# Kernel tuning notes

Measured on AMD Instinct MI355X. Metric: run time of the kernel, lower is better.

Reference implementation:

```python
import jax, jax.numpy as jnp
import numpy as np
from jax import lax

B, T, C_IN, HW = 16, 2048, 17, 8
N_CONV, HID, OUT = 4, 150, 2
IN_SZ = N_CONV * 6 * 6  # 144


def setup_inputs() -> dict:
    key = jax.random.key(0)
    ks = jax.random.split(key, 9)
    s = lambda *sh: 1.0 / np.sqrt(sh[-1])
    return {
        "inputs": jax.random.normal(ks[0], (B, T, C_IN, HW, HW), jnp.float32),
        "conv_w": jax.random.normal(ks[1], (N_CONV, C_IN, 3, 3), jnp.float32) * 0.1,
        "conv_b": jax.random.normal(ks[2], (N_CONV,), jnp.float32) * 0.1,
        "w_ih": jax.random.normal(ks[3], (4 * HID, IN_SZ), jnp.float32) * s(IN_SZ),
        "w_hh": jax.random.normal(ks[4], (4 * HID, HID), jnp.float32) * s(HID),
        "b_ih": jax.random.normal(ks[5], (4 * HID,), jnp.float32) * s(HID),
        "b_hh": jax.random.normal(ks[6], (4 * HID,), jnp.float32) * s(HID),
        "last_w": jax.random.normal(ks[7], (OUT, HID), jnp.float32) * s(HID),
        "last_b": jax.random.normal(ks[8], (OUT,), jnp.float32) * s(HID),
    }


def reference(inputs, conv_w, conv_b, w_ih, w_hh, b_ih, b_hh, last_w, last_b):
    b, t = inputs.shape[:2]
    # Conv2d over all timesteps at once (same math as the per-step loop).
    x = inputs.reshape(b * t, C_IN, HW, HW)
    y = lax.conv_general_dilated(
        x, conv_w, window_strides=(1, 1), padding="VALID",
        dimension_numbers=("NCHW", "OIHW", "NCHW"),
    ) + conv_b[None, :, None, None]           # [B*T, 4, 6, 6]
    y = jax.nn.relu(y).reshape(b, t, IN_SZ)   # [B, T, 144]
    # Precompute input-to-gate projection for every step (batched GEMM).
    gates_x = jnp.einsum("btf,gf->btg", y, w_ih) + b_ih + b_hh  # [B, T, 600]

    def step(carry, gx):
        h, c = carry
        g = gx + h @ w_hh.T  # [B, 600]; PyTorch gate order: i, f, g, o
        i, f, gg, o = jnp.split(g, 4, axis=-1)
        c = jax.nn.sigmoid(f) * c + jax.nn.sigmoid(i) * jnp.tanh(gg)
        h = jax.nn.sigmoid(o) * jnp.tanh(c)
        return (h, c), None

    h0 = jnp.zeros((b, HID), inputs.dtype)
    (hT, _), _ = lax.scan(step, (h0, h0), jnp.swapaxes(gates_x, 0, 1))
    return hT @ last_w.T + last_b  # [B, 2] == last(h_T).squeeze()
```

## Files before the change

### kernel.cpp

```cpp
#include <hip/hip_runtime.h>

typedef _Float16 f16;
typedef _Float16 f16x4 __attribute__((ext_vector_type(4)));
typedef _Float16 f16x8 __attribute__((ext_vector_type(8)));
typedef float f32x4 __attribute__((ext_vector_type(4)));
typedef int i32x4 __attribute__((ext_vector_type(4)));

#define TLEN 2048
#define TPAD 2050
#define NCOL 640
#define GSTEP (16 * NCOL)
#define SPITCH 1099
#define K1 1.4426950408889634f
#define K2 2.8853900817779268f

__global__ __launch_bounds__(64) void rowmax_k(const float* __restrict__ w_hh,
                                               float* __restrict__ rowmax)
{
    const int r = blockIdx.x * 64 + threadIdx.x;
    if (r < 600) {
        float m = 0.f;
        for (int k = 0; k < 150; ++k) m = fmaxf(m, fabsf(w_hh[r * 150 + k]));
        rowmax[r] = m;
    }
}

__global__ void prep_weights(const float* __restrict__ w_ih,
                             const float* __restrict__ w_hh,
                             const float* __restrict__ b_ih,
                             const float* __restrict__ b_hh,
                             const float* __restrict__ rowmax,
                             f16* __restrict__ wihf, signed char* __restrict__ whhq,
                             float* __restrict__ biasp, float* __restrict__ dsc)
{
    const int idx = blockIdx.x * blockDim.x + threadIdx.x;
    const int stride = gridDim.x * blockDim.x;
    for (int i = idx; i < 40 * 5 * 64 * 8; i += stride) {
        const int e = i & 7;
        const int lane = (i >> 3) & 63;
        const int kt = (i >> 9) % 5;
        const int nt = i / 2560;
        const int colg = nt * 16 + (lane & 15);
        const int u = colg >> 2, G = colg & 3;
        const int k = kt * 32 + (lane >> 4) * 8 + e;
        const float sc = (G == 2) ? K2 : -K1;
        f16 vi = (f16)0.f;
        if (u < 150 && k < 144) vi = (f16)(w_ih[(G * 150 + u) * 144 + k] * sc);
        wihf[i] = vi;
    }
    for (int i = idx; i < 40 * 3 * 64 * 16; i += stride) {
        const int byte = i & 15;
        const int lane = (i >> 4) & 63;
        const int kt = (i >> 10) % 3;
        const int nt = i / 3072;
        const int colg = nt * 16 + (lane & 15);
        const int u = colg >> 2, G = colg & 3;
        const int k = kt * 64 + (lane >> 4) * 16 + byte;
        signed char q = 0;
        if (u < 150 && k < 150) {
            const int row = G * 150 + u;
            const float rm = rowmax[row];
            if (rm > 0.f)
                q = (signed char)(int)rintf(w_hh[row * 150 + k] * (127.f / rm));
        }
        whhq[i] = q;
    }
    for (int i = idx; i < NCOL; i += stride) {
        const int u = i >> 2, G = i & 3;
        const float sc = (G == 2) ? K2 : -K1;
        biasp[i] = (u < 150) ? (b_ih[G * 150 + u] + b_hh[G * 150 + u]) * sc : 0.f;
        dsc[i]   = (u < 150) ? sc * rowmax[G * 150 + u] * (1.f / 16129.f) : 0.f;
    }
}

__global__ __launch_bounds__(512, 1) void conv_gemm(
    const float* __restrict__ inp, const float* __restrict__ cw,
    const float* __restrict__ cb,
    const f16* __restrict__ wihf, const float* __restrict__ biasp,
    f16* __restrict__ gates3)
{
    __shared__ float s_in[16][SPITCH];
    __shared__ __align__(16) f16 s_y[8][16][168];
    __shared__ float s_w[612];
    const int tid = threadIdx.x, w = tid >> 6, lane = tid & 63;
    const int col = lane & 15, grp = lane >> 4;
    for (int i = tid; i < 612; i += 512) s_w[i] = cw[i];

    f16x8 bfr[5][5];
    float bb[5];
    #pragma unroll
    for (int i = 0; i < 5; ++i) {
        const int nt = w * 5 + i;
        const f16* wf = wihf + (size_t)(nt * 5) * 512;
        #pragma unroll
        for (int kt = 0; kt < 5; ++kt)
            bfr[i][kt] = *(const f16x8*)(wf + kt * 512 + lane * 8);
        bb[i] = biasp[nt * 16 + col];
    }
    const int cb_b = tid & 15, unit = tid >> 4;
    const int oc = unit / 6, oy = unit % 6;
    const float cbias = (unit < 24) ? cb[oc] : 0.f;
    __syncthreads();

    const int t0 = blockIdx.x * 8;
    for (int tl = 0; tl < 8; ++tl) {
        const int t = t0 + tl;
        __syncthreads();
        {
            const int si = tid >> 5, l2 = tid & 31;
            const float* ip = inp + ((size_t)si * TLEN + t) * 1088;
            for (int k = l2; k < 1088; k += 32) s_in[si][k] = ip[k];
        }
        __syncthreads();
        if (unit < 24) {
            const float* wp = s_w + oc * 153;
            float acc[6] = {cbias, cbias, cbias, cbias, cbias, cbias};
            #pragma unroll 1
            for (int ic = 0; ic < 17; ++ic) {
                const float* rowb = &s_in[cb_b][ic * 64 + oy * 8];
                #pragma unroll
                for (int ky = 0; ky < 3; ++ky) {
                    const float* r = rowb + ky * 8;
                    const float w0 = wp[ic * 9 + ky * 3 + 0];
                    const float w1 = wp[ic * 9 + ky * 3 + 1];
                    const float w2 = wp[ic * 9 + ky * 3 + 2];
                    #pragma unroll
                    for (int ox = 0; ox < 6; ++ox)
                        acc[ox] += r[ox] * w0 + r[ox + 1] * w1 + r[ox + 2] * w2;
                }
            }
            #pragma unroll
            for (int ox = 0; ox < 6; ++ox)
                s_y[tl][cb_b][oc * 36 + oy * 6 + ox] = (f16)fmaxf(acc[ox], 0.f);
        } else if (unit == 24) {
            #pragma unroll
            for (int k = 0; k < 16; ++k) s_y[tl][cb_b][144 + k] = (f16)0.f;
        }
    }
    __syncthreads();
    for (int tl = 0; tl < 8; ++tl) {
        const int t = t0 + tl;
        f16x8 a[5];
        #pragma unroll
        for (int kt = 0; kt < 5; ++kt)
            a[kt] = *(const f16x8*)(&s_y[tl][col][kt * 32 + grp * 8]);
        #pragma unroll
        for (int i = 0; i < 5; ++i) {
            f32x4 acc = {0.f, 0.f, 0.f, 0.f};
            #pragma unroll
            for (int kt = 0; kt < 5; ++kt)
                acc = __builtin_amdgcn_mfma_f32_16x16x32_f16(a[kt], bfr[i][kt], acc, 0, 0, 0);
            const int colg = (w * 5 + i) * 16 + col;
            #pragma unroll
            for (int r = 0; r < 4; ++r)
                gates3[((size_t)(t * 16 + grp * 4 + r)) * NCOL + colg] =
                    (f16)(acc[r] + bb[i]);
        }
    }
}

__device__ __forceinline__ void lstm_stepQ(
    int t, int cur, f16x4& pfu, f16x4& pfc, const f16*& pLoad,
    const i32x4 (&afrag)[5][3], const f32x4& scv,
    signed char* hqs, f16* hfs, float& cst,
    int grp, int sel, bool wr, int u)
{
    const f16x4 pnew = *(const f16x4*)pLoad;
    pLoad += GSTEP;

    const signed char* hr = hqs + cur * 192 + grp * 16;
    i32x4 bf[3];
    #pragma unroll
    for (int kt = 0; kt < 3; ++kt)
        bf[kt] = *(const i32x4*)(hr + kt * 64);

    float gx0 = (float)pfu[0], gx1 = (float)pfu[1];
    float gx2 = (float)pfu[2], gx3 = (float)pfu[3];
    pfc = pnew;

    const i32x4 zc = {0, 0, 0, 0};
    i32x4 acc[5];
    #pragma unroll
    for (int i = 0; i < 5; ++i)
        acc[i] = __builtin_amdgcn_mfma_i32_16x16x64_i8(afrag[i][0], bf[0], zc, 0, 0, 0);
    #pragma unroll
    for (int kt = 1; kt < 3; ++kt)
        #pragma unroll
        for (int i = 0; i < 5; ++i)
            acc[i] = __builtin_amdgcn_mfma_i32_16x16x64_i8(afrag[i][kt], bf[kt], acc[i], 0, 0, 0);

    int s0 = acc[0][0], s1 = acc[0][1], s2 = acc[0][2], s3 = acc[0][3];
    #pragma unroll
    for (int i = 1; i < 5; ++i) {
        const bool p = (sel == i);
        s0 = p ? acc[i][0] : s0;
        s1 = p ? acc[i][1] : s1;
        s2 = p ? acc[i][2] : s2;
        s3 = p ? acc[i][3] : s3;
    }

    const float g0 = fmaf((float)s0, scv[0], gx0);
    const float g1 = fmaf((float)s1, scv[1], gx1);
    const float g2 = fmaf((float)s2, scv[2], gx2);
    const float g3 = fmaf((float)s3, scv[3], gx3);

    const float ei = __builtin_amdgcn_exp2f(g0);
    const float ef = __builtin_amdgcn_exp2f(g1);
    const float eg = __builtin_amdgcn_exp2f(fminf(g2, 38.f));
    const float eo = __builtin_amdgcn_exp2f(g3);
    const float dig = (1.f + ei) * (eg + 1.f);
    const float c = cst * __builtin_amdgcn_rcpf(1.f + ef)
                  + (eg - 1.f) * __builtin_amdgcn_rcpf(dig);
    cst = c;
    const float ec = __builtin_amdgcn_exp2f(fminf(K2 * c, 80.f));
    const float h = (ec - 1.f) * __builtin_amdgcn_rcpf((1.f + eo) * (ec + 1.f));

    if (wr) hqs[(cur ^ 1) * 192 + u] = (signed char)(int)rintf(127.f * h);
    if (t == TLEN - 1 && wr) hfs[u] = (f16)h;

    asm volatile("s_waitcnt lgkmcnt(0)" ::: "memory");
    __builtin_amdgcn_s_barrier();
    __builtin_amdgcn_sched_barrier(0);
}

__global__ __launch_bounds__(512, 1) void lstm_scan(
    const f16* __restrict__ gates3, const signed char* __restrict__ whhq,
    const float* __restrict__ dsc,
    const float* __restrict__ last_w, const float* __restrict__ last_b,
    float* __restrict__ out)
{
    __shared__ __align__(16) signed char hq[2 * 192];
    __shared__ __align__(16) f16 hf[160];
    const int b = blockIdx.x;
    const int tid = threadIdx.x, w = tid >> 6, lane = tid & 63;
    const int col = lane & 15, grp = lane >> 4;
    const int sel = (col < 5) ? col : ((col < 10) ? col - 5 : ((col < 15) ? col - 10 : 0));
    const bool wr = (col < 5);
    const int u = 20 * w + 4 * sel + grp;

    for (int i = tid; i < 2 * 192; i += 512) hq[i] = 0;

    i32x4 afrag[5][3];
    #pragma unroll
    for (int i = 0; i < 5; ++i)
        #pragma unroll
        for (int kt = 0; kt < 3; ++kt)
            afrag[i][kt] =
                *(const i32x4*)(whhq + (size_t)(((5 * w + i) * 3 + kt) * 64 + lane) * 16);

    const f32x4 scv = *(const f32x4*)(dsc + 4 * u);
    float cst = 0.f;
    __syncthreads();

    const f16* gbu = gates3 + (size_t)b * NCOL + 80 * w + 16 * sel + 4 * grp;
    f16x4 pA = *(const f16x4*)(gbu);
    f16x4 pB = *(const f16x4*)(gbu + (size_t)1 * GSTEP);
    const f16* pLoad = gbu + (size_t)2 * GSTEP;

    #pragma unroll 1
    for (int tb = 0; tb < TLEN; tb += 2) {
        lstm_stepQ(tb,     0, pA, pA, pLoad, afrag, scv, hq, hf, cst, grp, sel, wr, u);
        lstm_stepQ(tb + 1, 1, pB, pB, pLoad, afrag, scv, hq, hf, cst, grp, sel, wr, u);
    }

    if (tid < 2) {
        float s = last_b[tid];
        for (int j = 0; j < 150; ++j)
            s += (float)hf[j] * last_w[tid * 150 + j];
        out[b * 2 + tid] = s;
    }
}

extern "C" void kernel_launch(void* const* d_in, const int* in_sizes, int n_in,
                              void* d_out, int out_size, void* d_ws, size_t ws_size,
                              hipStream_t stream) {
    const float* inp    = (const float*)d_in[0];
    const float* conv_w = (const float*)d_in[1];
    const float* conv_b = (const float*)d_in[2];
    const float* w_ih   = (const float*)d_in[3];
    const float* w_hh   = (const float*)d_in[4];
    const float* b_ih   = (const float*)d_in[5];
    const float* b_hh   = (const float*)d_in[6];
    const float* last_w = (const float*)d_in[7];
    const float* last_b = (const float*)d_in[8];
    float* out = (float*)d_out;

    char* ws = (char*)d_ws;
    size_t off = 0;
    f16*   gates3 = (f16*)(ws + off);  off += (size_t)TPAD * 16 * NCOL * 2;
    f16*   wihf   = (f16*)(ws + off);  off += 204800;
    signed char* whhq = (signed char*)(ws + off); off += 122880;
    float* biasp  = (float*)(ws + off); off += 2560;
    float* dsc    = (float*)(ws + off); off += 2560;
    float* rowmax = (float*)(ws + off); off += 2560;

    rowmax_k<<<10, 64, 0, stream>>>(w_hh, rowmax);
    prep_weights<<<120, 256, 0, stream>>>(w_ih, w_hh, b_ih, b_hh, rowmax,
                                          wihf, whhq, biasp, dsc);
    conv_gemm<<<256, 512, 0, stream>>>(inp, conv_w, conv_b, wihf, biasp, gates3);
    lstm_scan<<<16, 512, 0, stream>>>(gates3, whhq, dsc, last_w, last_b, out);
}
```

Before: 1.004 ms.

## Fold weight prep kernels into conv_gemm and lstm_scan, vectorize conv loads

Removes the separate rowmax and weight-prep launches. Each conv_gemm block now converts w_ih and the biases to f16 fragments itself, and each lstm_scan block computes the w_hh row maxima and int8-quantizes its fragments on entry. This saves two kernel launches and the workspace round trips. The conv input staging and the stencil reads switch to float4 accesses, with the shared pitch padded to 1100 to keep 16-byte alignment. The cost is redundant weight conversion in every block, which adds latency at the start of the serial LSTM kernel, and a possible rise in shared-memory bank conflicts from the new pitch.

```diff
diff --git a/kernel.cpp b/kernel.cpp
--- a/kernel.cpp
+++ b/kernel.cpp
@@ -10,76 +10,18 @@
 #define TPAD 2050
 #define NCOL 640
 #define GSTEP (16 * NCOL)
-#define SPITCH 1099
+#define SPITCH 1100
 #define K1 1.4426950408889634f
 #define K2 2.8853900817779268f
-
-__global__ __launch_bounds__(64) void rowmax_k(const float* __restrict__ w_hh,
-                                               float* __restrict__ rowmax)
-{
-    const int r = blockIdx.x * 64 + threadIdx.x;
-    if (r < 600) {
-        float m = 0.f;
-        for (int k = 0; k < 150; ++k) m = fmaxf(m, fabsf(w_hh[r * 150 + k]));
-        rowmax[r] = m;
-    }
-}
-
-__global__ void prep_weights(const float* __restrict__ w_ih,
-                             const float* __restrict__ w_hh,
-                             const float* __restrict__ b_ih,
-                             const float* __restrict__ b_hh,
-                             const float* __restrict__ rowmax,
-                             f16* __restrict__ wihf, signed char* __restrict__ whhq,
-                             float* __restrict__ biasp, float* __restrict__ dsc)
-{
-    const int idx = blockIdx.x * blockDim.x + threadIdx.x;
-    const int stride = gridDim.x * blockDim.x;
-    for (int i = idx; i < 40 * 5 * 64 * 8; i += stride) {
-        const int e = i & 7;
-        const int lane = (i >> 3) & 63;
-        const int kt = (i >> 9) % 5;
-        const int nt = i / 2560;
-        const int colg = nt * 16 + (lane & 15);
-        const int u = colg >> 2, G = colg & 3;
-        const int k = kt * 32 + (lane >> 4) * 8 + e;
-        const float sc = (G == 2) ? K2 : -K1;
-        f16 vi = (f16)0.f;
-        if (u < 150 && k < 144) vi = (f16)(w_ih[(G * 150 + u) * 144 + k] * sc);
-        wihf[i] = vi;
-    }
-    for (int i = idx; i < 40 * 3 * 64 * 16; i += stride) {
-        const int byte = i & 15;
-        const int lane = (i >> 4) & 63;
-        const int kt = (i >> 10) % 3;
-        const int nt = i / 3072;
-        const int colg = nt * 16 + (lane & 15);
-        const int u = colg >> 2, G = colg & 3;
-        const int k = kt * 64 + (lane >> 4) * 16 + byte;
-        signed char q = 0;
-        if (u < 150 && k < 150) {
-            const int row = G * 150 + u;
-            const float rm = rowmax[row];
-            if (rm > 0.f)
-                q = (signed char)(int)rintf(w_hh[row * 150 + k] * (127.f / rm));
-        }
-        whhq[i] = q;
-    }
-    for (int i = idx; i < NCOL; i += stride) {
-        const int u = i >> 2, G = i & 3;
-        const float sc = (G == 2) ? K2 : -K1;
-        biasp[i] = (u < 150) ? (b_ih[G * 150 + u] + b_hh[G * 150 + u]) * sc : 0.f;
-        dsc[i]   = (u < 150) ? sc * rowmax[G * 150 + u] * (1.f / 16129.f) : 0.f;
-    }
-}
 
 __global__ __launch_bounds__(512, 1) void conv_gemm(
     const float* __restrict__ inp, const float* __restrict__ cw,
     const float* __restrict__ cb,
-    const f16* __restrict__ wihf, const float* __restrict__ biasp,
+    const float* __restrict__ w_ih, const float* __restrict__ b_ih,
+    const float* __restrict__ b_hh,
     f16* __restrict__ gates3)
 {
-    __shared__ float s_in[16][SPITCH];
+    __shared__ __align__(16) float s_in[16][SPITCH];
     __shared__ __align__(16) f16 s_y[8][16][168];
     __shared__ float s_w[612];
     const int tid = threadIdx.x, w = tid >> 6, lane = tid & 63;
@@ -90,13 +32,27 @@
     float bb[5];
     #pragma unroll
     for (int i = 0; i < 5; ++i) {
-        const int nt = w * 5 + i;
-        const f16* wf = wihf + (size_t)(nt * 5) * 512;
-        #pragma unroll
-        for (int kt = 0; kt < 5; ++kt)
-            bfr[i][kt] = *(const f16x8*)(wf + kt * 512 + lane * 8);
-        bb[i] = biasp[nt * 16 + col];
-    }
+        const int colg = (w * 5 + i) * 16 + col;
+        const int u = colg >> 2, G = colg & 3;
+        const float sc = (G == 2) ? K2 : -K1;
+        const bool valid = (u < 150);
+        const int row = valid ? G * 150 + u : 0;
+        #pragma unroll
+        for (int kt = 0; kt < 5; ++kt) {
+            const int k0 = kt * 32 + grp * 8;
+            f16x8 v;
+            #pragma unroll
+            for (int e = 0; e < 8; ++e) v[e] = (f16)0.f;
+            if (valid && k0 < 144) {
+                const float* p = w_ih + (size_t)row * 144 + k0;
+                #pragma unroll
+                for (int e = 0; e < 8; ++e) v[e] = (f16)(p[e] * sc);
+            }
+            bfr[i][kt] = v;
+        }
+        bb[i] = valid ? (b_ih[row] + b_hh[row]) * sc : 0.f;
+    }
+
     const int cb_b = tid & 15, unit = tid >> 4;
     const int oc = unit / 6, oy = unit % 6;
     const float cbias = (unit < 24) ? cb[oc] : 0.f;
@@ -108,8 +64,10 @@
         __syncthreads();
         {
             const int si = tid >> 5, l2 = tid & 31;
-            const float* ip = inp + ((size_t)si * TLEN + t) * 1088;
-            for (int k = l2; k < 1088; k += 32) s_in[si][k] = ip[k];
+            const float4* ip =
+                (const float4*)(inp + ((size_t)si * TLEN + t) * 1088);
+            for (int k = l2; k < 272; k += 32)
+                *(float4*)(&s_in[si][k * 4]) = ip[k];
         }
         __syncthreads();
         if (unit < 24) {
@@ -117,16 +75,20 @@
             float acc[6] = {cbias, cbias, cbias, cbias, cbias, cbias};
             #pragma unroll 1
             for (int ic = 0; ic < 17; ++ic) {
-                const float* rowb = &s_in[cb_b][ic * 64 + oy * 8];
                 #pragma unroll
                 for (int ky = 0; ky < 3; ++ky) {
-                    const float* r = rowb + ky * 8;
+                    const float* r = &s_in[cb_b][ic * 64 + (oy + ky) * 8];
+                    const float4 f0 = *(const float4*)r;
+                    const float4 f1 = *(const float4*)(r + 4);
                     const float w0 = wp[ic * 9 + ky * 3 + 0];
                     const float w1 = wp[ic * 9 + ky * 3 + 1];
                     const float w2 = wp[ic * 9 + ky * 3 + 2];
-                    #pragma unroll
-                    for (int ox = 0; ox < 6; ++ox)
-                        acc[ox] += r[ox] * w0 + r[ox + 1] * w1 + r[ox + 2] * w2;
+                    acc[0] += f0.x * w0 + f0.y * w1 + f0.z * w2;
+                    acc[1] += f0.y * w0 + f0.z * w1 + f0.w * w2;
+                    acc[2] += f0.z * w0 + f0.w * w1 + f1.x * w2;
+                    acc[3] += f0.w * w0 + f1.x * w1 + f1.y * w2;
+                    acc[4] += f1.x * w0 + f1.y * w1 + f1.z * w2;
+                    acc[5] += f1.y * w0 + f1.z * w1 + f1.w * w2;
                 }
             }
             #pragma unroll
@@ -224,13 +186,13 @@
 }
 
 __global__ __launch_bounds__(512, 1) void lstm_scan(
-    const f16* __restrict__ gates3, const signed char* __restrict__ whhq,
-    const float* __restrict__ dsc,
+    const f16* __restrict__ gates3, const float* __restrict__ w_hh,
     const float* __restrict__ last_w, const float* __restrict__ last_b,
     float* __restrict__ out)
 {
     __shared__ __align__(16) signed char hq[2 * 192];
     __shared__ __align__(16) f16 hf[160];
+    __shared__ float s_rm[600];
     const int b = blockIdx.x;
     const int tid = threadIdx.x, w = tid >> 6, lane = tid & 63;
     const int col = lane & 15, grp = lane >> 4;
@@ -240,15 +202,50 @@
 
     for (int i = tid; i < 2 * 192; i += 512) hq[i] = 0;
 
+    for (int r = tid; r < 600; r += 512) {
+        const float* p = w_hh + (size_t)r * 150;
+        float m = 0.f;
+        for (int k = 0; k < 150; k += 2) {
+            m = fmaxf(m, fabsf(p[k]));
+            m = fmaxf(m, fabsf(p[k + 1]));
+        }
+        s_rm[r] = m;
+    }
+    __syncthreads();
+
     i32x4 afrag[5][3];
     #pragma unroll
-    for (int i = 0; i < 5; ++i)
-        #pragma unroll
-        for (int kt = 0; kt < 3; ++kt)
-            afrag[i][kt] =
-                *(const i32x4*)(whhq + (size_t)(((5 * w + i) * 3 + kt) * 64 + lane) * 16);
-
-    const f32x4 scv = *(const f32x4*)(dsc + 4 * u);
+    for (int i = 0; i < 5; ++i) {
+        const int colg = (5 * w + i) * 16 + col;
+        const int uu = colg >> 2, G = colg & 3;
+        const bool valid = (uu < 150);
+        const int row = valid ? G * 150 + uu : 0;
+        const float rm = s_rm[row];
+        const float qs = (valid && rm > 0.f) ? 127.f / rm : 0.f;
+        const float* p = w_hh + (size_t)row * 150;
+        #pragma unroll
+        for (int kt = 0; kt < 3; ++kt) {
+            int wv[4] = {0, 0, 0, 0};
+            #pragma unroll
+            for (int byte = 0; byte < 16; ++byte) {
+                const int k = kt * 64 + grp * 16 + byte;
+                int q = 0;
+                if (k < 150) q = (int)rintf(p[k] * qs);
+                wv[byte >> 2] |= (q & 255) << ((byte & 3) * 8);
+            }
+            afrag[i][kt] = (i32x4){wv[0], wv[1], wv[2], wv[3]};
+        }
+    }
+    f32x4 scv;
+    {
+        const bool vu = (u < 150);
+        #pragma unroll
+        for (int G = 0; G < 4; ++G) {
+            const float sc = (G == 2) ? K2 : -K1;
+            const int idx = vu ? G * 150 + u : 0;
+            scv[G] = vu ? sc * s_rm[idx] * (1.f / 16129.f) : 0.f;
+        }
+    }
     float cst = 0.f;
     __syncthreads();
 
@@ -285,18 +282,8 @@
     const float* last_b = (const float*)d_in[8];
     float* out = (float*)d_out;
 
-    char* ws = (char*)d_ws;
-    size_t off = 0;
-    f16*   gates3 = (f16*)(ws + off);  off += (size_t)TPAD * 16 * NCOL * 2;
-    f16*   wihf   = (f16*)(ws + off);  off += 204800;
-    signed char* whhq = (signed char*)(ws + off); off += 122880;
-    float* biasp  = (float*)(ws + off); off += 2560;
-    float* dsc    = (float*)(ws + off); off += 2560;
-    float* rowmax = (float*)(ws + off); off += 2560;
-
-    rowmax_k<<<10, 64, 0, stream>>>(w_hh, rowmax);
-    prep_weights<<<120, 256, 0, stream>>>(w_ih, w_hh, b_ih, b_hh, rowmax,
-                                          wihf, whhq, biasp, dsc);
-    conv_gemm<<<256, 512, 0, stream>>>(inp, conv_w, conv_b, wihf, biasp, gates3);
-    lstm_scan<<<16, 512, 0, stream>>>(gates3, whhq, dsc, last_w, last_b, out);
-}
+    f16* gates3 = (f16*)d_ws;
+
+    conv_gemm<<<256, 512, 0, stream>>>(inp, conv_w, conv_b, w_ih, b_ih, b_hh, gates3);
+    lstm_scan<<<16, 512, 0, stream>>>(gates3, w_hh, last_w, last_b, out);
+}
```

Result: no change. 1.004 ms (+0.1%).
